# Kernel tuning notes

Hardware: AMD Instinct MI355X
Metric: run time of the kernel (lower is better)

Reference implementation:

```python
import jax, jax.numpy as jnp
import numpy as np

B, N, F, H, D = 2, 2048, 1024, 16, 64


def setup_inputs() -> dict:
    key = jax.random.key(0)
    ks = jax.random.split(key, 5)
    s = 0.02
    return {
        "x": jax.random.normal(ks[0], (B, N, F), jnp.float32),
        "w_qkv": (jax.random.normal(ks[1], (3 * H * D, F), jnp.float32) * s),
        "w_out": (jax.random.normal(ks[2], (F, H * D), jnp.float32) * s),
        "w_hp_pre": (jax.random.normal(ks[3], (H, H), jnp.float32) * (1.0 / H)),
        "b_hp_pre": jnp.zeros((H,), jnp.float32),
        "w_hp_post": (jax.random.normal(ks[4], (H, H), jnp.float32) * (1.0 / H)),
        "b_hp_post": jnp.zeros((H,), jnp.float32),
    }


def reference(x, w_qkv, w_out, w_hp_pre, b_hp_pre, w_hp_post, b_hp_post):
    b, n, f = x.shape
    # qkv projection; rearrange 'b n (h d qkv) -> qkv b h n d' (qkv innermost)
    proj = (x @ w_qkv.T).reshape(b, n, H, D, 3)
    q = jnp.transpose(proj[..., 0], (0, 2, 1, 3))  # b h n d
    k = jnp.transpose(proj[..., 1], (0, 2, 1, 3))
    v = jnp.transpose(proj[..., 2], (0, 2, 1, 3))
    kv = jnp.stack([k, v], axis=0)  # (2, b, h, n, d) -- returned cache

    scale = D ** -0.5
    dots = jnp.einsum('bhid,bhjd->bhij', q, k) * scale
    # pre talking-heads: 1x1 conv over head channel
    dots = jnp.einsum('gh,bhij->bgij', w_hp_pre, dots) + b_hp_pre[None, :, None, None]
    attn = jax.nn.softmax(dots, axis=-1)
    # post talking-heads
    attn = jnp.einsum('gh,bhij->bgij', w_hp_post, attn) + b_hp_post[None, :, None, None]
    out = jnp.einsum('bhij,bhjd->bhid', attn, v)
    out = jnp.transpose(out, (0, 2, 1, 3)).reshape(b, n, H * D)
    out = out @ w_out.T
    return out, kv
```

## Files before the change

### kernel.cpp

```cpp
#include <hip/hip_runtime.h>
#include <hip/hip_bf16.h>
#include <cstdint>
#include <cstddef>

#define B_ 2
#define N_ 2048
#define F_ 1024
#define H_ 16
#define D_ 64

typedef float f32x4 __attribute__((ext_vector_type(4)));
typedef short s16x8 __attribute__((ext_vector_type(8)));
typedef short s16x4 __attribute__((ext_vector_type(4)));

__device__ __forceinline__ unsigned short f2bf(float f) {
  union { __hip_bfloat16 h; unsigned short u; } c;
  c.h = __float2bfloat16(f);
  return c.u;
}

__device__ __forceinline__ void bar_lgkm() {
  asm volatile("s_waitcnt lgkmcnt(0)" ::: "memory");
  __builtin_amdgcn_s_barrier();
}

__global__ __launch_bounds__(256) void cvt_bf16(const float* __restrict__ in,
                                                unsigned short* __restrict__ out,
                                                int n8) {
  const int t = blockIdx.x * 256 + threadIdx.x;
  if (t >= n8) return;
  const float4* p = (const float4*)in + (size_t)t * 2;
  float4 a = p[0], b = p[1];
  s16x8 o;
  o[0] = f2bf(a.x); o[1] = f2bf(a.y); o[2] = f2bf(a.z); o[3] = f2bf(a.w);
  o[4] = f2bf(b.x); o[5] = f2bf(b.y); o[6] = f2bf(b.z); o[7] = f2bf(b.w);
  *((s16x8*)out + t) = o;
}

__global__ __launch_bounds__(256) void cvt_wqkv_perm(const float* __restrict__ in,
                                                     unsigned short* __restrict__ out) {
  const int t = blockIdx.x * 256 + threadIdx.x;
  const int rowp = t >> 7;
  const int kk = (t & 127) * 8;
  const int c = rowp >> 10, rem = rowp & 1023;
  const int h = rem >> 6, d = rem & 63;
  const float* p = in + (size_t)(h * 192 + d * 3 + c) * 1024 + kk;
  float4 a = *(const float4*)p, b = *(const float4*)(p + 4);
  s16x8 o;
  o[0] = f2bf(a.x); o[1] = f2bf(a.y); o[2] = f2bf(a.z); o[3] = f2bf(a.w);
  o[4] = f2bf(b.x); o[5] = f2bf(b.y); o[6] = f2bf(b.z); o[7] = f2bf(b.w);
  *((s16x8*)&out[(size_t)rowp * 1024 + kk]) = o;
}

__global__ __launch_bounds__(256) void cvt_sum4(const float* __restrict__ a,
                                                unsigned short* __restrict__ out) {
  const int t = blockIdx.x * 256 + threadIdx.x;
  const size_t stride = (size_t)B_ * N_ * 1024 / 4;
  float4 x0 = *((const float4*)a + t);
  float4 x1 = *((const float4*)a + stride + t);
  float4 x2 = *((const float4*)a + 2 * stride + t);
  float4 x3 = *((const float4*)a + 3 * stride + t);
  s16x4 o;
  o[0] = f2bf((x0.x + x1.x) + (x2.x + x3.x));
  o[1] = f2bf((x0.y + x1.y) + (x2.y + x3.y));
  o[2] = f2bf((x0.z + x1.z) + (x2.z + x3.z));
  o[3] = f2bf((x0.w + x1.w) + (x2.w + x3.w));
  *((s16x4*)out + t) = o;
}

template <int MODE>
__global__ __launch_bounds__(256) void gemm_bf16(const unsigned short* __restrict__ A,
                                                 const unsigned short* __restrict__ W,
                                                 float* __restrict__ o0,
                                                 unsigned short* __restrict__ oQ,
                                                 unsigned short* __restrict__ oK,
                                                 unsigned short* __restrict__ oVt) {
  __shared__ unsigned short As[128 * 72];
  __shared__ unsigned short Bs[128 * 72];
  const int m0 = blockIdx.y * 128, c0 = blockIdx.x * 128;
  const int tid = threadIdx.x;
  const int wave = tid >> 6, lane = tid & 63;
  const int wm = (wave & 1) * 64, wn = (wave >> 1) * 64;
  const int lm = lane & 15, lq = lane >> 4;
  f32x4 acc[4][4] = {};
  for (int k0 = 0; k0 < 1024; k0 += 64) {
#pragma unroll
    for (int it = 0; it < 4; ++it) {
      const int chunk = it * 256 + tid;
      const int row = chunk >> 3, kq = (chunk & 7) * 8;
      *(float4*)&As[row * 72 + kq] = *(const float4*)&A[(size_t)(m0 + row) * 1024 + k0 + kq];
      *(float4*)&Bs[row * 72 + kq] = *(const float4*)&W[(size_t)(c0 + row) * 1024 + k0 + kq];
    }
    __syncthreads();
#pragma unroll
    for (int ks = 0; ks < 2; ++ks) {
      s16x8 af[4], bfr[4];
#pragma unroll
      for (int i = 0; i < 4; ++i) {
        af[i] = *(const s16x8*)&As[(wm + i * 16 + lm) * 72 + ks * 32 + lq * 8];
        bfr[i] = *(const s16x8*)&Bs[(wn + i * 16 + lm) * 72 + ks * 32 + lq * 8];
      }
#pragma unroll
      for (int i = 0; i < 4; ++i)
#pragma unroll
        for (int j = 0; j < 4; ++j)
          acc[i][j] = __builtin_amdgcn_mfma_f32_16x16x32_bf16(af[i], bfr[j], acc[i][j], 0, 0, 0);
    }
    __syncthreads();
  }
  if (MODE == 1) {
#pragma unroll
    for (int i = 0; i < 4; ++i)
#pragma unroll
      for (int j = 0; j < 4; ++j)
#pragma unroll
        for (int r = 0; r < 4; ++r) {
          const int m = m0 + wm + i * 16 + lq * 4 + r;
          const int col = c0 + wn + j * 16 + lm;
          o0[(size_t)m * 1024 + col] = acc[i][j][r];
        }
  } else {
    const int cls = blockIdx.x >> 3;
    const int colbase = (blockIdx.x & 7) * 128;
    if (cls == 0) {
#pragma unroll
      for (int i = 0; i < 4; ++i)
#pragma unroll
        for (int j = 0; j < 4; ++j) {
          const int cl = colbase + wn + j * 16 + lm;
          const int h = cl >> 6, d = cl & 63;
#pragma unroll
          for (int r = 0; r < 4; ++r) {
            const int m = m0 + wm + i * 16 + lq * 4 + r;
            const int bb = m >> 11, n = m & 2047;
            oQ[(((size_t)bb * H_ + h) * N_ + n) * D_ + d] = f2bf(acc[i][j][r]);
          }
        }
    } else if (cls == 1) {
#pragma unroll
      for (int i = 0; i < 4; ++i)
#pragma unroll
        for (int j = 0; j < 4; ++j) {
          const int cl = colbase + wn + j * 16 + lm;
          const int h = cl >> 6, d = cl & 63;
#pragma unroll
          for (int r = 0; r < 4; ++r) {
            const int m = m0 + wm + i * 16 + lq * 4 + r;
            const int bb = m >> 11, n = m & 2047;
            const size_t idx = (((size_t)bb * H_ + h) * N_ + n) * D_ + d;
            o0[idx] = acc[i][j][r];
            oK[idx] = f2bf(acc[i][j][r]);
          }
        }
    } else {
#pragma unroll
      for (int i = 0; i < 4; ++i) {
        const int n0 = m0 + wm + i * 16 + lq * 4;
        const int bb = n0 >> 11, nl = n0 & 2047;
#pragma unroll
        for (int j = 0; j < 4; ++j) {
          const int cl = colbase + wn + j * 16 + lm;
          const int h = cl >> 6, d = cl & 63;
          s16x4 vp;
#pragma unroll
          for (int r = 0; r < 4; ++r) {
            const size_t idx = (((size_t)bb * H_ + h) * N_ + nl + r) * D_ + d;
            o0[(size_t)B_ * H_ * N_ * D_ + idx] = acc[i][j][r];
            vp[r] = (short)f2bf(acc[i][j][r]);
          }
          *(s16x4*)&oVt[(((size_t)bb * H_ + h) * D_ + d) * N_ + nl] = vp;
        }
      }
    }
  }
}

#define SS_J 20
#define SLOT 320
#define SS_I 644
#define SS_HALF (32 * SS_I + 16)
#define PS_J 36
#define PS_G 1156
#define PS_HALF (16 * PS_G)

__device__ __forceinline__ f32x4 mfma16(s16x8 a, s16x8 b, f32x4 c) {
  return __builtin_amdgcn_mfma_f32_16x16x32_bf16(a, b, c, 0, 0, 0);
}

__device__ __forceinline__ void load_k(s16x8 (&kr)[2][2][2],
                                       const unsigned short* __restrict__ Kb,
                                       int b, int h0, int j0, int lm, int lq) {
#pragma unroll
  for (int jt = 0; jt < 2; ++jt)
#pragma unroll
    for (int hh = 0; hh < 2; ++hh) {
      const unsigned short* kp =
          &Kb[(((size_t)(b * H_ + h0 + hh) * N_) + j0 + jt * 16 + lm) * D_ + lq * 8];
      kr[jt][hh][0] = *(const s16x8*)kp;
      kr[jt][hh][1] = *(const s16x8*)(kp + 32);
    }
}

__device__ __forceinline__ void load_v(s16x8 (&vt)[2][4],
                                       const unsigned short* __restrict__ Vt,
                                       int b, int h0, int j0, int lm, int lq) {
#pragma unroll
  for (int g = 0; g < 2; ++g)
#pragma unroll
    for (int nd = 0; nd < 4; ++nd)
      vt[g][nd] = *(const s16x8*)&Vt[(((size_t)(b * H_ + h0 + g) * D_) + nd * 16 + lm) * N_ + j0 + lq * 8];
}

__device__ __forceinline__ void scores_phase(const s16x8 (&aq)[2][2][2],
                                             const s16x8 (&kr)[2][2][2],
                                             unsigned short* Sb,
                                             int lm, int lq, int h0) {
#pragma unroll
  for (int jt = 0; jt < 2; ++jt) {
    f32x4 c[2][2];
    __builtin_amdgcn_s_setprio(1);
#pragma unroll
    for (int hh = 0; hh < 2; ++hh)
#pragma unroll
      for (int mi = 0; mi < 2; ++mi) {
        f32x4 cc = {};
        cc = mfma16(aq[hh][mi][0], kr[jt][hh][0], cc);
        cc = mfma16(aq[hh][mi][1], kr[jt][hh][1], cc);
        c[hh][mi] = cc;
      }
    __builtin_amdgcn_s_setprio(0);
#pragma unroll
    for (int mi = 0; mi < 2; ++mi)
#pragma unroll
      for (int r = 0; r < 4; ++r) {
        unsigned int pk = (unsigned int)f2bf(c[0][mi][r]) | ((unsigned int)f2bf(c[1][mi][r]) << 16);
        *(unsigned int*)&Sb[(mi * 16 + lq * 4 + r) * SS_I + jt * SLOT + lm * SS_J + h0] = pk;
      }
  }
}

__global__ __launch_bounds__(512, 4) void attn_l(const unsigned short* __restrict__ Qb,
                                                 const unsigned short* __restrict__ Kb,
                                                 const float* __restrict__ wpre,
                                                 const float* __restrict__ bpre,
                                                 float* __restrict__ l_glob) {
  __shared__ unsigned short Ssh[SS_HALF];
  const int tid = threadIdx.x;
  const int wave = tid >> 6, lane = tid & 63;
  const int lm = lane & 15, lq = lane >> 4;
  const int b = blockIdx.z, jh = blockIdx.y;
  const int i0 = blockIdx.x * 32;
  const int j00 = jh * 512;
  const int h0 = wave * 2;

  for (int t = tid; t < SS_HALF; t += 512) Ssh[t] = 0;

  s16x8 aq[2][2][2];
#pragma unroll
  for (int hh = 0; hh < 2; ++hh)
#pragma unroll
    for (int mi = 0; mi < 2; ++mi)
#pragma unroll
      for (int ks = 0; ks < 2; ++ks)
        aq[hh][mi][ks] = *(const s16x8*)&Qb[(((size_t)(b * H_ + h0 + hh) * N_) + i0 + mi * 16 + lm) * D_ + ks * 32 + lq * 8];

  s16x8 apre;
#pragma unroll
  for (int t = 0; t < 8; ++t) apre[t] = 0;
  if (lq < 2)
#pragma unroll
    for (int t = 0; t < 8; ++t) apre[t] = (short)f2bf(wpre[lm * 16 + lq * 8 + t] * 0.125f);
  float bpre_r[4];
#pragma unroll
  for (int r = 0; r < 4; ++r) bpre_r[r] = bpre[lq * 4 + r];

  float lacc[4][4] = {};

  s16x8 kr[2][2][2];
  load_k(kr, Kb, b, h0, j00, lm, lq);

  for (int t = 0; t < 16; ++t) {
    bar_lgkm();
    scores_phase(aq, kr, Ssh, lm, lq, h0);
    const int jn = j00 + (t + 1 < 16 ? (t + 1) * 32 : 480);
    load_k(kr, Kb, b, h0, jn, lm, lq);
    bar_lgkm();
#pragma unroll
    for (int jt = 0; jt < 2; ++jt) {
      s16x4 p0[4], p1[4];
#pragma unroll
      for (int u = 0; u < 4; ++u) {
        const unsigned short* srow = &Ssh[(wave * 4 + u) * SS_I + jt * SLOT + lm * SS_J + lq * 8];
        p0[u] = *(const s16x4*)srow;
        p1[u] = *(const s16x4*)(srow + 4);
      }
#pragma unroll
      for (int u = 0; u < 4; ++u) {
        s16x8 bs;
        bs[0] = p0[u][0]; bs[1] = p0[u][1]; bs[2] = p0[u][2]; bs[3] = p0[u][3];
        bs[4] = p1[u][0]; bs[5] = p1[u][1]; bs[6] = p1[u][2]; bs[7] = p1[u][3];
        f32x4 c = {};
        c = mfma16(apre, bs, c);
#pragma unroll
        for (int r = 0; r < 4; ++r) lacc[u][r] += __expf(c[r] + bpre_r[r]);
      }
    }
  }
#pragma unroll
  for (int ig = 0; ig < 4; ++ig)
#pragma unroll
    for (int r = 0; r < 4; ++r) {
      float v = lacc[ig][r];
      v += __shfl_xor(v, 1); v += __shfl_xor(v, 2);
      v += __shfl_xor(v, 4); v += __shfl_xor(v, 8);
      if (lm == 0)
        atomicAdd(&l_glob[((size_t)b * N_ + i0 + wave * 4 + ig) * H_ + lq * 4 + r], v);
    }
}

__global__ __launch_bounds__(512, 2) void attn_av(const unsigned short* __restrict__ Qb,
                                                  const unsigned short* __restrict__ Kb,
                                                  const unsigned short* __restrict__ Vt,
                                                  const float* __restrict__ wpre,
                                                  const float* __restrict__ bpre,
                                                  const float* __restrict__ wpost,
                                                  const float* __restrict__ bpost,
                                                  const float* __restrict__ l_glob,
                                                  float* __restrict__ Opart) {
  __shared__ unsigned short Ssh[2 * SS_HALF];
  __shared__ unsigned short Psh[2 * PS_HALF];
  __shared__ float linv[512];
  const int tid = threadIdx.x;
  const int wave = tid >> 6, lane = tid & 63;
  const int lm = lane & 15, lq = lane >> 4;
  const int b = blockIdx.z, jh = blockIdx.y;
  const int i0 = blockIdx.x * 32;
  const int j00 = jh * 512;
  const int h0 = wave * 2;
  float* Oout = Opart + (size_t)jh * ((size_t)B_ * N_ * 1024);

  for (int t = tid; t < 2 * SS_HALF; t += 512) Ssh[t] = 0;
  linv[tid] = 1.0f / l_glob[((size_t)b * N_ + i0 + (tid >> 4)) * H_ + (tid & 15)];

  s16x8 aq[2][2][2];
#pragma unroll
  for (int hh = 0; hh < 2; ++hh)
#pragma unroll
    for (int mi = 0; mi < 2; ++mi)
#pragma unroll
      for (int ks = 0; ks < 2; ++ks)
        aq[hh][mi][ks] = *(const s16x8*)&Qb[(((size_t)(b * H_ + h0 + hh) * N_) + i0 + mi * 16 + lm) * D_ + ks * 32 + lq * 8];

  s16x8 apre, apost;
#pragma unroll
  for (int t = 0; t < 8; ++t) { apre[t] = 0; apost[t] = 0; }
  if (lq < 2)
#pragma unroll
    for (int t = 0; t < 8; ++t) {
      apre[t] = (short)f2bf(wpre[lm * 16 + lq * 8 + t] * 0.125f);
      apost[t] = (short)f2bf(wpost[lm * 16 + lq * 8 + t]);
    }
  float bpre_r[4];
#pragma unroll
  for (int r = 0; r < 4; ++r) bpre_r[r] = bpre[lq * 4 + r];
  const float bpost_lm = bpost[lm];

  const int bpA = ((((2 * lq) & 3) * 16 + lm) << 2);
  const int bpB = ((((2 * lq + 1) & 3) * 16 + lm) << 2);

  __syncthreads();

  float lifs[4][4];
#pragma unroll
  for (int u = 0; u < 4; ++u)
#pragma unroll
    for (int r = 0; r < 4; ++r)
      lifs[u][r] = linv[(wave * 4 + u) * 16 + lq * 4 + r];

  f32x4 acc[2][2][4] = {};

  s16x8 kr[2][2][2];
  load_k(kr, Kb, b, h0, j00, lm, lq);
  s16x8 vt[2][4];
  load_v(vt, Vt, b, h0, j00, lm, lq);
  scores_phase(aq, kr, &Ssh[0], lm, lq, h0);
  load_k(kr, Kb, b, h0, j00 + 32, lm, lq);
  bar_lgkm();

#pragma unroll 2
  for (int t = 0; t < 16; ++t) {
    unsigned short* Sc = &Ssh[(t & 1) * SS_HALF];
    unsigned short* Pc = &Psh[(t & 1) * PS_HALF];
#pragma unroll
    for (int jt = 0; jt < 2; ++jt) {
      s16x4 p0[4], p1[4];
#pragma unroll
      for (int u = 0; u < 4; ++u) {
        const unsigned short* srow = &Sc[(wave * 4 + u) * SS_I + jt * SLOT + lm * SS_J + lq * 8];
        p0[u] = *(const s16x4*)srow;
        p1[u] = *(const s16x4*)(srow + 4);
      }
      f32x4 cpre[4];
#pragma unroll
      for (int u = 0; u < 4; ++u) {
        s16x8 bs;
        bs[0] = p0[u][0]; bs[1] = p0[u][1]; bs[2] = p0[u][2]; bs[3] = p0[u][3];
        bs[4] = p1[u][0]; bs[5] = p1[u][1]; bs[6] = p1[u][2]; bs[7] = p1[u][3];
        f32x4 c = {};
        cpre[u] = mfma16(apre, bs, c);
      }
#pragma unroll
      for (int u = 0; u < 4; ++u) {
        float e0 = __expf(cpre[u][0] + bpre_r[0]) * lifs[u][0];
        float e1 = __expf(cpre[u][1] + bpre_r[1]) * lifs[u][1];
        float e2 = __expf(cpre[u][2] + bpre_r[2]) * lifs[u][2];
        float e3 = __expf(cpre[u][3] + bpre_r[3]) * lifs[u][3];
        int e01 = (int)((unsigned int)f2bf(e0) | ((unsigned int)f2bf(e1) << 16));
        int e23 = (int)((unsigned int)f2bf(e2) | ((unsigned int)f2bf(e3) << 16));
        union { int i[4]; s16x8 v; } cv;
        cv.i[0] = __builtin_amdgcn_ds_bpermute(bpA, e01);
        cv.i[1] = __builtin_amdgcn_ds_bpermute(bpA, e23);
        cv.i[2] = __builtin_amdgcn_ds_bpermute(bpB, e01);
        cv.i[3] = __builtin_amdgcn_ds_bpermute(bpB, e23);
        f32x4 c2 = {};
        c2 = mfma16(cv.v, apost, c2);
        s16x4 pv;
#pragma unroll
        for (int r = 0; r < 4; ++r) pv[r] = (short)f2bf(c2[r] + bpost_lm);
        *(s16x4*)&Pc[lm * PS_G + (wave * 4 + u) * PS_J + jt * 16 + lq * 4] = pv;
      }
    }
    if (t < 15) {
      scores_phase(aq, kr, &Ssh[((t + 1) & 1) * SS_HALF], lm, lq, h0);
      const int jn = j00 + (t + 2 < 16 ? (t + 2) * 32 : 480);
      load_k(kr, Kb, b, h0, jn, lm, lq);
    }
    bar_lgkm();
    s16x8 ap[2][2];
#pragma unroll
    for (int g = 0; g < 2; ++g)
#pragma unroll
      for (int mi = 0; mi < 2; ++mi) {
        const unsigned short* pb = &Pc[(h0 + g) * PS_G + (mi * 16 + lm) * PS_J + lq * 8];
        s16x4 a0 = *(const s16x4*)pb;
        s16x4 a1 = *(const s16x4*)(pb + 4);
        s16x8 tt;
        tt[0] = a0[0]; tt[1] = a0[1]; tt[2] = a0[2]; tt[3] = a0[3];
        tt[4] = a1[0]; tt[5] = a1[1]; tt[6] = a1[2]; tt[7] = a1[3];
        ap[g][mi] = tt;
      }
    __builtin_amdgcn_s_setprio(1);
#pragma unroll
    for (int g = 0; g < 2; ++g)
#pragma unroll
      for (int mi = 0; mi < 2; ++mi)
#pragma unroll
        for (int nd = 0; nd < 4; ++nd)
          acc[g][mi][nd] = mfma16(ap[g][mi], vt[g][nd], acc[g][mi][nd]);
    __builtin_amdgcn_s_setprio(0);
    const int jv = j00 + (t + 1 < 16 ? (t + 1) * 32 : 480);
    load_v(vt, Vt, b, h0, jv, lm, lq);
  }
#pragma unroll
  for (int g = 0; g < 2; ++g)
#pragma unroll
    for (int mi = 0; mi < 2; ++mi)
#pragma unroll
      for (int nd = 0; nd < 4; ++nd)
#pragma unroll
        for (int r = 0; r < 4; ++r)
          Oout[((size_t)b * N_ + i0 + mi * 16 + lq * 4 + r) * 1024 + (h0 + g) * 64 + nd * 16 + lm] = acc[g][mi][nd][r];
}

extern "C" void kernel_launch(void* const* d_in, const int* in_sizes, int n_in,
                              void* d_out, int out_size, void* d_ws,
                              size_t ws_size, hipStream_t stream) {
  (void)in_sizes; (void)n_in; (void)out_size; (void)ws_size;
  const float* x      = (const float*)d_in[0];
  const float* w_qkv  = (const float*)d_in[1];
  const float* w_out  = (const float*)d_in[2];
  const float* w_pre  = (const float*)d_in[3];
  const float* b_pre  = (const float*)d_in[4];
  const float* w_post = (const float*)d_in[5];
  const float* b_post = (const float*)d_in[6];

  float* out = (float*)d_out;
  float* kv  = out + (size_t)B_ * N_ * F_;

  unsigned short* xb  = (unsigned short*)d_ws;
  unsigned short* wqb = xb + (size_t)4096 * 1024;
  unsigned short* wob = wqb + (size_t)3072 * 1024;
  unsigned short* Qb  = wob + (size_t)1024 * 1024;
  unsigned short* Kb  = Qb + (size_t)B_ * H_ * N_ * D_;
  unsigned short* Vt  = Kb + (size_t)B_ * H_ * N_ * D_;
  unsigned short* O1  = Vt + (size_t)B_ * H_ * N_ * D_;
  float* l_glob = (float*)(O1 + (size_t)B_ * N_ * F_);
  float* Oh = l_glob + (size_t)B_ * N_ * H_;

  cvt_bf16<<<dim3(4096 * 1024 / 8 / 256), 256, 0, stream>>>(x, xb, 4096 * 1024 / 8);
  cvt_wqkv_perm<<<dim3(3072 * 128 / 256), 256, 0, stream>>>(w_qkv, wqb);
  cvt_bf16<<<dim3(1024 * 1024 / 8 / 256), 256, 0, stream>>>(w_out, wob, 1024 * 1024 / 8);
  hipMemsetAsync(l_glob, 0, (size_t)B_ * N_ * H_ * 4, stream);

  gemm_bf16<0><<<dim3(3072 / 128, 4096 / 128), 256, 0, stream>>>(xb, wqb, kv, Qb, Kb, Vt);

  attn_l<<<dim3(N_ / 32, 4, B_), 512, 0, stream>>>(Qb, Kb, w_pre, b_pre, l_glob);
  attn_av<<<dim3(N_ / 32, 4, B_), 512, 0, stream>>>(Qb, Kb, Vt, w_pre, b_pre, w_post, b_post,
                                                    l_glob, Oh);

  cvt_sum4<<<dim3(B_ * N_ * F_ / 4 / 256), 256, 0, stream>>>(Oh, O1);

  gemm_bf16<1><<<dim3(1024 / 128, 4096 / 128), 256, 0, stream>>>(O1, wob, out, nullptr, nullptr, nullptr);
}
```

Measured before the change: 383.8 us.

## Split attention work to one head per wave with 1024-thread blocks

Both attention kernels now assign a single head to each of 16 waves in a 1024-thread block, where before each of 8 waves handled two heads. Per-thread register arrays for Q, K, V, scores and accumulators are halved, and the talking-heads stages now cover two query rows per wave instead of four. The goal is more waves in flight to hide latency and lower register pressure. The cost is more barrier participants per block, 16-bit scattered LDS stores in place of packed 32-bit ones, and a launch bound of 1024x4 that may not be reachable with this LDS footprint.

```diff
diff --git a/kernel.cpp b/kernel.cpp
--- a/kernel.cpp
+++ b/kernel.cpp
@@ -187,63 +187,55 @@
   return __builtin_amdgcn_mfma_f32_16x16x32_bf16(a, b, c, 0, 0, 0);
 }
 
-__device__ __forceinline__ void load_k(s16x8 (&kr)[2][2][2],
-                                       const unsigned short* __restrict__ Kb,
-                                       int b, int h0, int j0, int lm, int lq) {
-#pragma unroll
-  for (int jt = 0; jt < 2; ++jt)
-#pragma unroll
-    for (int hh = 0; hh < 2; ++hh) {
-      const unsigned short* kp =
-          &Kb[(((size_t)(b * H_ + h0 + hh) * N_) + j0 + jt * 16 + lm) * D_ + lq * 8];
-      kr[jt][hh][0] = *(const s16x8*)kp;
-      kr[jt][hh][1] = *(const s16x8*)(kp + 32);
-    }
-}
-
-__device__ __forceinline__ void load_v(s16x8 (&vt)[2][4],
-                                       const unsigned short* __restrict__ Vt,
-                                       int b, int h0, int j0, int lm, int lq) {
-#pragma unroll
-  for (int g = 0; g < 2; ++g)
-#pragma unroll
-    for (int nd = 0; nd < 4; ++nd)
-      vt[g][nd] = *(const s16x8*)&Vt[(((size_t)(b * H_ + h0 + g) * D_) + nd * 16 + lm) * N_ + j0 + lq * 8];
-}
-
-__device__ __forceinline__ void scores_phase(const s16x8 (&aq)[2][2][2],
-                                             const s16x8 (&kr)[2][2][2],
-                                             unsigned short* Sb,
-                                             int lm, int lq, int h0) {
+__device__ __forceinline__ void load_k1(s16x8 (&kr)[2][2],
+                                        const unsigned short* __restrict__ Kb,
+                                        int b, int h0, int j0, int lm, int lq) {
 #pragma unroll
   for (int jt = 0; jt < 2; ++jt) {
-    f32x4 c[2][2];
+    const unsigned short* kp =
+        &Kb[(((size_t)(b * H_ + h0) * N_) + j0 + jt * 16 + lm) * D_ + lq * 8];
+    kr[jt][0] = *(const s16x8*)kp;
+    kr[jt][1] = *(const s16x8*)(kp + 32);
+  }
+}
+
+__device__ __forceinline__ void load_v1(s16x8 (&vt)[4],
+                                        const unsigned short* __restrict__ Vt,
+                                        int b, int h0, int j0, int lm, int lq) {
+#pragma unroll
+  for (int nd = 0; nd < 4; ++nd)
+    vt[nd] = *(const s16x8*)&Vt[(((size_t)(b * H_ + h0) * D_) + nd * 16 + lm) * N_ + j0 + lq * 8];
+}
+
+__device__ __forceinline__ void scores_phase1(const s16x8 (&aq)[2][2],
+                                              const s16x8 (&kr)[2][2],
+                                              unsigned short* Sb,
+                                              int lm, int lq, int h0) {
+#pragma unroll
+  for (int jt = 0; jt < 2; ++jt) {
+    f32x4 c[2];
     __builtin_amdgcn_s_setprio(1);
 #pragma unroll
-    for (int hh = 0; hh < 2; ++hh)
-#pragma unroll
-      for (int mi = 0; mi < 2; ++mi) {
-        f32x4 cc = {};
-        cc = mfma16(aq[hh][mi][0], kr[jt][hh][0], cc);
-        cc = mfma16(aq[hh][mi][1], kr[jt][hh][1], cc);
-        c[hh][mi] = cc;
-      }
+    for (int mi = 0; mi < 2; ++mi) {
+      f32x4 cc = {};
+      cc = mfma16(aq[mi][0], kr[jt][0], cc);
+      cc = mfma16(aq[mi][1], kr[jt][1], cc);
+      c[mi] = cc;
+    }
     __builtin_amdgcn_s_setprio(0);
 #pragma unroll
     for (int mi = 0; mi < 2; ++mi)
 #pragma unroll
-      for (int r = 0; r < 4; ++r) {
-        unsigned int pk = (unsigned int)f2bf(c[0][mi][r]) | ((unsigned int)f2bf(c[1][mi][r]) << 16);
-        *(unsigned int*)&Sb[(mi * 16 + lq * 4 + r) * SS_I + jt * SLOT + lm * SS_J + h0] = pk;
-      }
-  }
-}
-
-__global__ __launch_bounds__(512, 4) void attn_l(const unsigned short* __restrict__ Qb,
-                                                 const unsigned short* __restrict__ Kb,
-                                                 const float* __restrict__ wpre,
-                                                 const float* __restrict__ bpre,
-                                                 float* __restrict__ l_glob) {
+      for (int r = 0; r < 4; ++r)
+        Sb[(mi * 16 + lq * 4 + r) * SS_I + jt * SLOT + lm * SS_J + h0] = f2bf(c[mi][r]);
+  }
+}
+
+__global__ __launch_bounds__(1024, 4) void attn_l(const unsigned short* __restrict__ Qb,
+                                                  const unsigned short* __restrict__ Kb,
+                                                  const float* __restrict__ wpre,
+                                                  const float* __restrict__ bpre,
+                                                  float* __restrict__ l_glob) {
   __shared__ unsigned short Ssh[SS_HALF];
   const int tid = threadIdx.x;
   const int wave = tid >> 6, lane = tid & 63;
@@ -251,18 +243,16 @@
   const int b = blockIdx.z, jh = blockIdx.y;
   const int i0 = blockIdx.x * 32;
   const int j00 = jh * 512;
-  const int h0 = wave * 2;
-
-  for (int t = tid; t < SS_HALF; t += 512) Ssh[t] = 0;
-
-  s16x8 aq[2][2][2];
-#pragma unroll
-  for (int hh = 0; hh < 2; ++hh)
-#pragma unroll
-    for (int mi = 0; mi < 2; ++mi)
-#pragma unroll
-      for (int ks = 0; ks < 2; ++ks)
-        aq[hh][mi][ks] = *(const s16x8*)&Qb[(((size_t)(b * H_ + h0 + hh) * N_) + i0 + mi * 16 + lm) * D_ + ks * 32 + lq * 8];
+  const int h0 = wave;
+
+  for (int t = tid; t < SS_HALF; t += 1024) Ssh[t] = 0;
+
+  s16x8 aq[2][2];
+#pragma unroll
+  for (int mi = 0; mi < 2; ++mi)
+#pragma unroll
+    for (int ks = 0; ks < 2; ++ks)
+      aq[mi][ks] = *(const s16x8*)&Qb[(((size_t)(b * H_ + h0) * N_) + i0 + mi * 16 + lm) * D_ + ks * 32 + lq * 8];
 
   s16x8 apre;
 #pragma unroll
@@ -274,28 +264,28 @@
 #pragma unroll
   for (int r = 0; r < 4; ++r) bpre_r[r] = bpre[lq * 4 + r];
 
-  float lacc[4][4] = {};
-
-  s16x8 kr[2][2][2];
-  load_k(kr, Kb, b, h0, j00, lm, lq);
+  float lacc[2][4] = {};
+
+  s16x8 kr[2][2];
+  load_k1(kr, Kb, b, h0, j00, lm, lq);
 
   for (int t = 0; t < 16; ++t) {
     bar_lgkm();
-    scores_phase(aq, kr, Ssh, lm, lq, h0);
+    scores_phase1(aq, kr, Ssh, lm, lq, h0);
     const int jn = j00 + (t + 1 < 16 ? (t + 1) * 32 : 480);
-    load_k(kr, Kb, b, h0, jn, lm, lq);
+    load_k1(kr, Kb, b, h0, jn, lm, lq);
     bar_lgkm();
 #pragma unroll
     for (int jt = 0; jt < 2; ++jt) {
-      s16x4 p0[4], p1[4];
-#pragma unroll
-      for (int u = 0; u < 4; ++u) {
-        const unsigned short* srow = &Ssh[(wave * 4 + u) * SS_I + jt * SLOT + lm * SS_J + lq * 8];
+      s16x4 p0[2], p1[2];
+#pragma unroll
+      for (int u = 0; u < 2; ++u) {
+        const unsigned short* srow = &Ssh[(wave * 2 + u) * SS_I + jt * SLOT + lm * SS_J + lq * 8];
         p0[u] = *(const s16x4*)srow;
         p1[u] = *(const s16x4*)(srow + 4);
       }
 #pragma unroll
-      for (int u = 0; u < 4; ++u) {
+      for (int u = 0; u < 2; ++u) {
         s16x8 bs;
         bs[0] = p0[u][0]; bs[1] = p0[u][1]; bs[2] = p0[u][2]; bs[3] = p0[u][3];
         bs[4] = p1[u][0]; bs[5] = p1[u][1]; bs[6] = p1[u][2]; bs[7] = p1[u][3];
@@ -307,26 +297,26 @@
     }
   }
 #pragma unroll
-  for (int ig = 0; ig < 4; ++ig)
+  for (int ig = 0; ig < 2; ++ig)
 #pragma unroll
     for (int r = 0; r < 4; ++r) {
       float v = lacc[ig][r];
       v += __shfl_xor(v, 1); v += __shfl_xor(v, 2);
       v += __shfl_xor(v, 4); v += __shfl_xor(v, 8);
       if (lm == 0)
-        atomicAdd(&l_glob[((size_t)b * N_ + i0 + wave * 4 + ig) * H_ + lq * 4 + r], v);
-    }
-}
-
-__global__ __launch_bounds__(512, 2) void attn_av(const unsigned short* __restrict__ Qb,
-                                                  const unsigned short* __restrict__ Kb,
-                                                  const unsigned short* __restrict__ Vt,
-                                                  const float* __restrict__ wpre,
-                                                  const float* __restrict__ bpre,
-                                                  const float* __restrict__ wpost,
-                                                  const float* __restrict__ bpost,
-                                                  const float* __restrict__ l_glob,
-                                                  float* __restrict__ Opart) {
+        atomicAdd(&l_glob[((size_t)b * N_ + i0 + wave * 2 + ig) * H_ + lq * 4 + r], v);
+    }
+}
+
+__global__ __launch_bounds__(1024, 4) void attn_av(const unsigned short* __restrict__ Qb,
+                                                   const unsigned short* __restrict__ Kb,
+                                                   const unsigned short* __restrict__ Vt,
+                                                   const float* __restrict__ wpre,
+                                                   const float* __restrict__ bpre,
+                                                   const float* __restrict__ wpost,
+                                                   const float* __restrict__ bpost,
+                                                   const float* __restrict__ l_glob,
+                                                   float* __restrict__ Opart) {
   __shared__ unsigned short Ssh[2 * SS_HALF];
   __shared__ unsigned short Psh[2 * PS_HALF];
   __shared__ float linv[512];
@@ -336,20 +326,19 @@
   const int b = blockIdx.z, jh = blockIdx.y;
   const int i0 = blockIdx.x * 32;
   const int j00 = jh * 512;
-  const int h0 = wave * 2;
+  const int h0 = wave;
   float* Oout = Opart + (size_t)jh * ((size_t)B_ * N_ * 1024);
 
-  for (int t = tid; t < 2 * SS_HALF; t += 512) Ssh[t] = 0;
-  linv[tid] = 1.0f / l_glob[((size_t)b * N_ + i0 + (tid >> 4)) * H_ + (tid & 15)];
-
-  s16x8 aq[2][2][2];
-#pragma unroll
-  for (int hh = 0; hh < 2; ++hh)
-#pragma unroll
-    for (int mi = 0; mi < 2; ++mi)
-#pragma unroll
-      for (int ks = 0; ks < 2; ++ks)
-        aq[hh][mi][ks] = *(const s16x8*)&Qb[(((size_t)(b * H_ + h0 + hh) * N_) + i0 + mi * 16 + lm) * D_ + ks * 32 + lq * 8];
+  for (int t = tid; t < 2 * SS_HALF; t += 1024) Ssh[t] = 0;
+  if (tid < 512)
+    linv[tid] = 1.0f / l_glob[((size_t)b * N_ + i0 + (tid >> 4)) * H_ + (tid & 15)];
+
+  s16x8 aq[2][2];
+#pragma unroll
+  for (int mi = 0; mi < 2; ++mi)
+#pragma unroll
+    for (int ks = 0; ks < 2; ++ks)
+      aq[mi][ks] = *(const s16x8*)&Qb[(((size_t)(b * H_ + h0) * N_) + i0 + mi * 16 + lm) * D_ + ks * 32 + lq * 8];
 
   s16x8 apre, apost;
 #pragma unroll
@@ -370,21 +359,21 @@
 
   __syncthreads();
 
-  float lifs[4][4];
-#pragma unroll
-  for (int u = 0; u < 4; ++u)
+  float lifs[2][4];
+#pragma unroll
+  for (int u = 0; u < 2; ++u)
 #pragma unroll
     for (int r = 0; r < 4; ++r)
-      lifs[u][r] = linv[(wave * 4 + u) * 16 + lq * 4 + r];
-
-  f32x4 acc[2][2][4] = {};
-
-  s16x8 kr[2][2][2];
-  load_k(kr, Kb, b, h0, j00, lm, lq);
-  s16x8 vt[2][4];
-  load_v(vt, Vt, b, h0, j00, lm, lq);
-  scores_phase(aq, kr, &Ssh[0], lm, lq, h0);
-  load_k(kr, Kb, b, h0, j00 + 32, lm, lq);
+      lifs[u][r] = linv[(wave * 2 + u) * 16 + lq * 4 + r];
+
+  f32x4 acc[2][4] = {};
+
+  s16x8 kr[2][2];
+  load_k1(kr, Kb, b, h0, j00, lm, lq);
+  s16x8 vt[4];
+  load_v1(vt, Vt, b, h0, j00, lm, lq);
+  scores_phase1(aq, kr, &Ssh[0], lm, lq, h0);
+  load_k1(kr, Kb, b, h0, j00 + 32, lm, lq);
   bar_lgkm();
 
 #pragma unroll 2
@@ -393,16 +382,16 @@
     unsigned short* Pc = &Psh[(t & 1) * PS_HALF];
 #pragma unroll
     for (int jt = 0; jt < 2; ++jt) {
-      s16x4 p0[4], p1[4];
-#pragma unroll
-      for (int u = 0; u < 4; ++u) {
-        const unsigned short* srow = &Sc[(wave * 4 + u) * SS_I + jt * SLOT + lm * SS_J + lq * 8];
+      s16x4 p0[2], p1[2];
+#pragma unroll
+      for (int u = 0; u < 2; ++u) {
+        const unsigned short* srow = &Sc[(wave * 2 + u) * SS_I + jt * SLOT + lm * SS_J + lq * 8];
         p0[u] = *(const s16x4*)srow;
         p1[u] = *(const s16x4*)(srow + 4);
       }
-      f32x4 cpre[4];
-#pragma unroll
-      for (int u = 0; u < 4; ++u) {
+      f32x4 cpre[2];
+#pragma unroll
+      for (int u = 0; u < 2; ++u) {
         s16x8 bs;
         bs[0] = p0[u][0]; bs[1] = p0[u][1]; bs[2] = p0[u][2]; bs[3] = p0[u][3];
         bs[4] = p1[u][0]; bs[5] = p1[u][1]; bs[6] = p1[u][2]; bs[7] = p1[u][3];
@@ -410,7 +399,7 @@
         cpre[u] = mfma16(apre, bs, c);
       }
 #pragma unroll
-      for (int u = 0; u < 4; ++u) {
+      for (int u = 0; u < 2; ++u) {
         float e0 = __expf(cpre[u][0] + bpre_r[0]) * lifs[u][0];
         float e1 = __expf(cpre[u][1] + bpre_r[1]) * lifs[u][1];
         float e2 = __expf(cpre[u][2] + bpre_r[2]) * lifs[u][2];
@@ -427,49 +416,43 @@
         s16x4 pv;
 #pragma unroll
         for (int r = 0; r < 4; ++r) pv[r] = (short)f2bf(c2[r] + bpost_lm);
-        *(s16x4*)&Pc[lm * PS_G + (wave * 4 + u) * PS_J + jt * 16 + lq * 4] = pv;
+        *(s16x4*)&Pc[lm * PS_G + (wave * 2 + u) * PS_J + jt * 16 + lq * 4] = pv;
       }
     }
     if (t < 15) {
-      scores_phase(aq, kr, &Ssh[((t + 1) & 1) * SS_HALF], lm, lq, h0);
+      scores_phase1(aq, kr, &Ssh[((t + 1) & 1) * SS_HALF], lm, lq, h0);
       const int jn = j00 + (t + 2 < 16 ? (t + 2) * 32 : 480);
-      load_k(kr, Kb, b, h0, jn, lm, lq);
+      load_k1(kr, Kb, b, h0, jn, lm, lq);
     }
     bar_lgkm();
-    s16x8 ap[2][2];
-#pragma unroll
-    for (int g = 0; g < 2; ++g)
-#pragma unroll
-      for (int mi = 0; mi < 2; ++mi) {
-        const unsigned short* pb = &Pc[(h0 + g) * PS_G + (mi * 16 + lm) * PS_J + lq * 8];
-        s16x4 a0 = *(const s16x4*)pb;
-        s16x4 a1 = *(const s16x4*)(pb + 4);
-        s16x8 tt;
-        tt[0] = a0[0]; tt[1] = a0[1]; tt[2] = a0[2]; tt[3] = a0[3];
-        tt[4] = a1[0]; tt[5] = a1[1]; tt[6] = a1[2]; tt[7] = a1[3];
-        ap[g][mi] = tt;
-      }
+    s16x8 ap[2];
+#pragma unroll
+    for (int mi = 0; mi < 2; ++mi) {
+      const unsigned short* pb = &Pc[h0 * PS_G + (mi * 16 + lm) * PS_J + lq * 8];
+      s16x4 a0 = *(const s16x4*)pb;
+      s16x4 a1 = *(const s16x4*)(pb + 4);
+      s16x8 tt;
+      tt[0] = a0[0]; tt[1] = a0[1]; tt[2] = a0[2]; tt[3] = a0[3];
+      tt[4] = a1[0]; tt[5] = a1[1]; tt[6] = a1[2]; tt[7] = a1[3];
+      ap[mi] = tt;
+    }
     __builtin_amdgcn_s_setprio(1);
 #pragma unroll
-    for (int g = 0; g < 2; ++g)
-#pragma unroll
-      for (int mi = 0; mi < 2; ++mi)
-#pragma unroll
-        for (int nd = 0; nd < 4; ++nd)
-          acc[g][mi][nd] = mfma16(ap[g][mi], vt[g][nd], acc[g][mi][nd]);
+    for (int mi = 0; mi < 2; ++mi)
+#pragma unroll
+      for (int nd = 0; nd < 4; ++nd)
+        acc[mi][nd] = mfma16(ap[mi], vt[nd], acc[mi][nd]);
     __builtin_amdgcn_s_setprio(0);
     const int jv = j00 + (t + 1 < 16 ? (t + 1) * 32 : 480);
-    load_v(vt, Vt, b, h0, jv, lm, lq);
-  }
-#pragma unroll
-  for (int g = 0; g < 2; ++g)
-#pragma unroll
-    for (int mi = 0; mi < 2; ++mi)
-#pragma unroll
-      for (int nd = 0; nd < 4; ++nd)
-#pragma unroll
-        for (int r = 0; r < 4; ++r)
-          Oout[((size_t)b * N_ + i0 + mi * 16 + lq * 4 + r) * 1024 + (h0 + g) * 64 + nd * 16 + lm] = acc[g][mi][nd][r];
+    load_v1(vt, Vt, b, h0, jv, lm, lq);
+  }
+#pragma unroll
+  for (int mi = 0; mi < 2; ++mi)
+#pragma unroll
+    for (int nd = 0; nd < 4; ++nd)
+#pragma unroll
+      for (int r = 0; r < 4; ++r)
+        Oout[((size_t)b * N_ + i0 + mi * 16 + lq * 4 + r) * 1024 + h0 * 64 + nd * 16 + lm] = acc[mi][nd][r];
 }
 
 extern "C" void kernel_launch(void* const* d_in, const int* in_sizes, int n_in,
@@ -504,9 +487,9 @@
 
   gemm_bf16<0><<<dim3(3072 / 128, 4096 / 128), 256, 0, stream>>>(xb, wqb, kv, Qb, Kb, Vt);
 
-  attn_l<<<dim3(N_ / 32, 4, B_), 512, 0, stream>>>(Qb, Kb, w_pre, b_pre, l_glob);
-  attn_av<<<dim3(N_ / 32, 4, B_), 512, 0, stream>>>(Qb, Kb, Vt, w_pre, b_pre, w_post, b_post,
-                                                    l_glob, Oh);
+  attn_l<<<dim3(N_ / 32, 4, B_), 1024, 0, stream>>>(Qb, Kb, w_pre, b_pre, l_glob);
+  attn_av<<<dim3(N_ / 32, 4, B_), 1024, 0, stream>>>(Qb, Kb, Vt, w_pre, b_pre, w_post, b_post,
+                                                     l_glob, Oh);
 
   cvt_sum4<<<dim3(B_ * N_ * F_ / 4 / 256), 256, 0, stream>>>(Oh, O1);
 
```

Measured after the change: 383.1 us. Within noise of the previous version (-0.2%).
